# Kernel optimization log

Hardware: AMD Instinct MI355X
Metric: run time of the kernel (lower is better)

The kernel has to match this reference:

```python
import jax, jax.numpy as jnp
import numpy as np

BN_EPS = 1e-5
LEAKY_SLOPE = 0.1


def conv_bn_leaky(x, w, gamma, beta, mean, var, pad):
    # Conv2d(no bias) + BatchNorm2d(inference) + LeakyReLU(0.1), NCHW/OIHW
    y = jax.lax.conv_general_dilated(
        x, w, window_strides=(1, 1), padding=[(pad, pad), (pad, pad)],
        dimension_numbers=("NCHW", "OIHW", "NCHW"))
    scale = gamma / jnp.sqrt(var + BN_EPS)
    shift = beta - mean * scale
    y = y * scale[None, :, None, None] + shift[None, :, None, None]
    return jnp.where(y > 0, y, LEAKY_SLOPE * y)


def reorg(x, s=2):
    # vedanet Reorg: out[b, (a*s+d)*C + c, i, j] = x[b, c, i*s+a, j*s+d]
    B, C, H, W = x.shape
    Ho, Wo = H // s, W // s
    return x.reshape(B, C, Ho, s, Wo, s).transpose(0, 3, 5, 1, 2, 4).reshape(B, s * s * C, Ho, Wo)


def setup_inputs() -> dict:
    key = jax.random.key(0)
    ks = jax.random.split(key, 10)
    B, H, W = 32, 19, 19
    NC, NA = 20, 5
    return {
        "stage6": jax.random.normal(ks[0], (B, 1024, H, W), jnp.float32),
        "stage5": jax.random.normal(ks[1], (B, 512, 2 * H, 2 * W), jnp.float32),
        "w1": jax.random.normal(ks[2], (64, 512, 1, 1), jnp.float32) * 0.05,
        "g1": jnp.ones((64,), jnp.float32),
        "b1": jnp.zeros((64,), jnp.float32),
        "m1": jax.random.normal(ks[3], (64,), jnp.float32) * 0.1,
        "v1": jax.random.uniform(ks[4], (64,), jnp.float32, 0.5, 1.5),
        "w2": jax.random.normal(ks[5], (1024, 1280, 3, 3), jnp.float32) * 0.02,
        "g2": jnp.ones((1024,), jnp.float32),
        "b2": jnp.zeros((1024,), jnp.float32),
        "m2": jax.random.normal(ks[6], (1024,), jnp.float32) * 0.1,
        "v2": jax.random.uniform(ks[7], (1024,), jnp.float32, 0.5, 1.5),
        "meta_state": jax.random.normal(ks[8], (NC, NA * 6, 1025), jnp.float32) * 0.05,
    }


def reference(stage6, stage5, w1, g1, b1, m1, v1, w2, g2, b2, m2, v2, meta_state):
    # layers[0]: 1x1 conv-bn-leaky on stage5, then Reorg(2) -> (B, 256, H, W)
    x = conv_bn_leaky(stage5, w1, g1, b1, m1, v1, pad=0)
    x = reorg(x, 2)
    # layers[1]: 3x3 conv-bn-leaky on concat -> (B, 1024, H, W)
    pre = conv_bn_leaky(jnp.concatenate([x, stage6], axis=1), w2, g2, b2, m2, v2, pad=1)
    # meta_predict: per-class 1x1 conv, batched as one einsum
    cls_w = meta_state[:, :, :-1]   # (NC, NA*6, 1024)
    cls_b = meta_state[:, :, -1]    # (NC, NA*6)
    out = jnp.einsum("bkij,cmk->bcmij", pre, cls_w) + cls_b[None, :, :, None, None]
    B, NC, M = pre.shape[0], meta_state.shape[0], meta_state.shape[1]
    return out.reshape(B * NC, M, pre.shape[2], pre.shape[3])
```

## Files before the change

### kernel.cpp

```cpp
#include <hip/hip_runtime.h>

typedef unsigned short u16;
typedef unsigned int   u32;

typedef __attribute__((ext_vector_type(8))) short bf16x8;
typedef __attribute__((ext_vector_type(4))) float f32x4;

__device__ __forceinline__ u16 f2bf(float f) {
  u32 u = __float_as_uint(f);
  u32 r = (u + 0x7fffu + ((u >> 16) & 1u)) >> 16;
  return (u16)r;
}

__device__ __forceinline__ void async16(const void* g, void* l) {
  __builtin_amdgcn_global_load_lds(
      (const __attribute__((address_space(1))) u32*)g,
      (__attribute__((address_space(3))) u32*)l, 16, 0, 0);
}

__global__ __launch_bounds__(256) void mega_prep_kern(
    const float* __restrict__ stage5, const float* __restrict__ s6,
    const float* __restrict__ w1,
    const float* __restrict__ g1, const float* __restrict__ b1,
    const float* __restrict__ m1, const float* __restrict__ v1,
    const float* __restrict__ w2, const float* __restrict__ g2,
    const float* __restrict__ b2, const float* __restrict__ m2,
    const float* __restrict__ v2, const float* __restrict__ meta,
    u16* __restrict__ in_bf, u16* __restrict__ w2p,
    u16* __restrict__ clsp, float* __restrict__ clsb,
    float* __restrict__ shift2)
{
  __shared__ __align__(16) char smem[18816];
  const int bid = blockIdx.x;
  const int t = threadIdx.x;

  if (bid < 722) {
    float* sc_s = (float*)smem;
    float* sh_s = (float*)(smem + 256);
    char*  aT   = smem + 512;
    char*  bT   = smem + 4608;
    const int w = t >> 6, lane = t & 63;
    if (t < 64) {
      float s = g1[t] * rsqrtf(v1[t] + 1e-5f);
      sc_s[t] = s;
      sh_s[t] = b1[t] - m1[t] * s;
    }
    const int m0 = bid * 64;
    const int pS = t & 63, gS = t >> 6;
    const int mS = m0 + pS;
    const int bS = mS / 1444, hwS = mS - bS * 1444;
    const float* s5 = stage5 + (size_t)bS * (512 * 1444) + hwS;
    const int ocA = t >> 2, icqA = t & 3;
    const float* w1r = w1 + (size_t)ocA * 512 + icqA * 8;
    char* aW = aT + (ocA >> 4) * 1024 + (icqA * 16 + (ocA & 15)) * 16;
    char* bW = bT + pS * 64 + ((gS ^ ((pS >> 1) & 3))) * 16;
    const int bR = (w * 16 + (lane & 15)) * 64 +
                   (((lane >> 4) ^ (((lane & 15) >> 1) & 3))) * 16;
    f32x4 acc[4] = {};
    __syncthreads();
    const float sA = sc_s[ocA];
    for (int kc = 0; kc < 16; ++kc) {
      const int ic0 = kc * 32;
      float a8[8], b8[8];
#pragma unroll
      for (int e = 0; e < 8; ++e) a8[e] = w1r[ic0 + e];
#pragma unroll
      for (int e = 0; e < 8; ++e) b8[e] = s5[(size_t)(ic0 + gS * 8 + e) * 1444];
      __syncthreads();
      uint4 av, bv;
      av.x = (u32)f2bf(a8[0] * sA) | ((u32)f2bf(a8[1] * sA) << 16);
      av.y = (u32)f2bf(a8[2] * sA) | ((u32)f2bf(a8[3] * sA) << 16);
      av.z = (u32)f2bf(a8[4] * sA) | ((u32)f2bf(a8[5] * sA) << 16);
      av.w = (u32)f2bf(a8[6] * sA) | ((u32)f2bf(a8[7] * sA) << 16);
      bv.x = (u32)f2bf(b8[0]) | ((u32)f2bf(b8[1]) << 16);
      bv.y = (u32)f2bf(b8[2]) | ((u32)f2bf(b8[3]) << 16);
      bv.z = (u32)f2bf(b8[4]) | ((u32)f2bf(b8[5]) << 16);
      bv.w = (u32)f2bf(b8[6]) | ((u32)f2bf(b8[7]) << 16);
      *(uint4*)aW = av;
      *(uint4*)bW = bv;
      __syncthreads();
      bf16x8 bfv = *(const bf16x8*)(bT + bR);
#pragma unroll
      for (int i = 0; i < 4; ++i) {
        bf16x8 af = *(const bf16x8*)(aT + i * 1024 + lane * 16);
        acc[i] = __builtin_amdgcn_mfma_f32_16x16x32_bf16(af, bfv, acc[i], 0, 0, 0);
      }
    }
    const int mE = m0 + w * 16 + (lane & 15);
    const int bE = mE / 1444, hwE = mE - bE * 1444;
    const int h = hwE / 38, wq = hwE - h * 38;
    const int ho = h >> 1, wo = wq >> 1, q = ((h & 1) << 1) | (wq & 1);
    u16* dst = in_bf + (((size_t)bE * 21 + 1 + ho) * 21 + 1 + wo) * 1280 + q * 64;
    const int lq = lane >> 4;
#pragma unroll
    for (int i = 0; i < 4; ++i) {
      int oc = i * 16 + lq * 4;
      float v0 = acc[i][0] + sh_s[oc + 0]; v0 = v0 > 0.f ? v0 : 0.1f * v0;
      float v1_ = acc[i][1] + sh_s[oc + 1]; v1_ = v1_ > 0.f ? v1_ : 0.1f * v1_;
      float v2_ = acc[i][2] + sh_s[oc + 2]; v2_ = v2_ > 0.f ? v2_ : 0.1f * v2_;
      float v3 = acc[i][3] + sh_s[oc + 3]; v3 = v3 > 0.f ? v3 : 0.1f * v3;
      u32 lo = (u32)f2bf(v0) | ((u32)f2bf(v1_) << 16);
      u32 hi = (u32)f2bf(v2_) | ((u32)f2bf(v3) << 16);
      u32* dp = (u32*)(dst + oc);
      dp[0] = lo; dp[1] = hi;
    }
    return;
  }

  if (bid < 3794) {
    u16 (*tile)[66] = (u16(*)[66])smem;
    const int sub = bid - 722;
    const int jt = sub % 6, ct = (sub / 6) % 16, b = sub / 96;
    const int ij0 = jt * 64, c0 = ct * 64;
    const int col = t & 63, rr = t >> 6;
#pragma unroll
    for (int r = 0; r < 16; ++r) {
      int cl = r * 4 + rr;
      int ij = ij0 + col;
      float v = 0.f;
      if (ij < 361) v = s6[((size_t)b * 1024 + c0 + cl) * 361 + ij];
      tile[cl][col] = f2bf(v);
    }
    __syncthreads();
#pragma unroll
    for (int r = 0; r < 16; ++r) {
      int ijl = r * 4 + rr;
      int ij = ij0 + ijl;
      if (ij < 361) {
        int i = ij / 19, j = ij - i * 19;
        in_bf[(((size_t)b * 21 + 1 + i) * 21 + 1 + j) * 1280 + 256 + c0 + col] =
            tile[col][ijl];
      }
    }
    return;
  }

  if (bid < 5394) {
    int gi = (bid - 3794) * 256 + t;
    int b = gi / 12800;
    int rem = gi - b * 12800;
    int p = rem / 160, qq = rem - p * 160;
    int row, col;
    if (p < 21)      { row = 0;      col = p; }
    else if (p < 42) { row = 20;     col = p - 21; }
    else if (p < 61) { row = p - 41; col = 0; }
    else             { row = p - 60; col = 20; }
    uint4 z = {0u, 0u, 0u, 0u};
    *(uint4*)(in_bf + (((size_t)b * 21 + row) * 21 + col) * 1280 + qq * 8) = z;
    return;
  }

  if (bid < 5694) {
    int idx = (bid - 5394) * 256 + t;
    int cm = idx >> 7, a = idx & 127;
    int kc = a >> 2, ksub = a & 3;
    int tile_ = cm >> 7, g = (cm >> 4) & 7, mm = cm & 15;
    const float* srcp = meta + (size_t)cm * 1025 + a * 8;
    uint4 v;
    v.x = (u32)f2bf(srcp[0]) | ((u32)f2bf(srcp[1]) << 16);
    v.y = (u32)f2bf(srcp[2]) | ((u32)f2bf(srcp[3]) << 16);
    v.z = (u32)f2bf(srcp[4]) | ((u32)f2bf(srcp[5]) << 16);
    v.w = (u32)f2bf(srcp[6]) | ((u32)f2bf(srcp[7]) << 16);
    size_t dst = (((size_t)tile_ * 32 + kc) * 8 + g) * 512
                 + (size_t)(ksub * 16 + mm) * 8;
    *(uint4*)(clsp + dst) = v;
    if (idx < 600) clsb[idx] = meta[(size_t)idx * 1025 + 1024];
    if (idx < 1024) {
      float sc = g2[idx] * rsqrtf(v2[idx] + 1e-5f);
      shift2[idx] = b2[idx] - m2[idx] * sc;
    }
    return;
  }

  {
    u16* tile = (u16*)smem;
    float* sc_s = (float*)(smem + 18720);
    const int sub = bid - 5694;
    const int icb = sub % 10;
    const int oc0 = (sub / 10) * 8;
    if (t < 8) sc_s[t] = g2[oc0 + t] * rsqrtf(v2[oc0 + t] + 1e-5f);
    __syncthreads();
    const float* src = w2 + (size_t)oc0 * 11520 + (size_t)icb * 128 * 9;
#pragma unroll
    for (int r = 0; r < 36; ++r) {
      int p = r * 256 + t;
      int oc_l = p / 1152, rem = p - oc_l * 1152;
      int ic_l = rem / 9, khw = rem - ic_l * 9;
      tile[oc_l * 1170 + khw * 130 + ic_l] =
          f2bf(src[(size_t)oc_l * 11520 + rem] * sc_s[oc_l]);
    }
    __syncthreads();
#pragma unroll
    for (int r = 0; r < 5; ++r) {
      int wi = r * 256 + t;
      if (wi < 1152) {
        int oc_l = wi / 144, q = wi - oc_l * 144;
        int khw = q >> 4, c = (q >> 2) & 3, ksub = q & 3;
        int oc = oc0 + oc_l;
        int kt = khw * 40 + icb * 4 + c;
        const u16* s = &tile[oc_l * 1170 + khw * 130 + c * 32 + ksub * 8];
        uint4 v;
        v.x = (u32)s[0] | ((u32)s[1] << 16);
        v.y = (u32)s[2] | ((u32)s[3] << 16);
        v.z = (u32)s[4] | ((u32)s[5] << 16);
        v.w = (u32)s[6] | ((u32)s[7] << 16);
        size_t dst = (((size_t)(oc >> 8) * 360 + kt) * 2 + ((oc & 255) >> 7)) * 4096
                     + (size_t)(((oc >> 4) & 7) * 64 + ksub * 16 + (oc & 15)) * 8;
        *(uint4*)(w2p + dst) = v;
      }
    }
  }
}

__global__ __launch_bounds__(512, 2) void conv2_gemm_kern(
    const u16* __restrict__ Wp, const u16* __restrict__ Ig,
    const float* __restrict__ shift2, u16* __restrict__ pre)
{
  __shared__ u16 As[2][16384];
  __shared__ u16 Bs[2][12288];
  __shared__ float shft[256];

  const int t = threadIdx.x;
  const int w = t >> 6, lane = t & 63;
  const int wm = w >> 2, wn = w & 3;

  const int xcd = blockIdx.x & 7, sub8 = blockIdx.x >> 3;
  const int s = (xcd < 4 ? xcd * 31 : 124 + (xcd - 4) * 30) + sub8;
  const int mTile = s >> 2, ocTile = s & 3;
  const int m0 = mTile * 192, oc0 = ocTile * 256;

  const int rw = t >> 2;
  const int rpart = ((t & 3) ^ ((t >> 3) & 3)) * 8;
  int mA = m0 + rw;        if (mA > 11551) mA = 11551;
  int mB = m0 + 128 + rw;  if (mB > 11551) mB = 11551;
  const int bA = mA / 361, ijA = mA - bA * 361;
  const int ohA = ijA / 19, owA = ijA - ohA * 19;
  const int bB = mB / 361, ijB = mB - bB * 361;
  const int ohB = ijB / 19, owB = ijB - ohB * 19;
  const u16* pI0 = Ig + (size_t)((bA * 21 + ohA) * 21 + owA) * 1280 + rpart;
  const u16* pI1 = Ig + (size_t)((bB * 21 + ohB) * 21 + owB) * 1280 + rpart;

  const u16* pW = Wp + (size_t)ocTile * 2949120 + (size_t)t * 8;

  const int aOff = wm * 4096 + lane * 8;
  const int bOff = (wn * 48 + (lane & 15)) * 32 +
                   (((lane >> 4) ^ ((lane >> 1) & 3)) * 8);

  async16(pW,                 &As[0][t * 8]);
  async16(pW + 4096,          &As[0][4096 + t * 8]);
  async16(pW + 8192,          &As[0][8192 + t * 8]);
  async16(pW + 12288,         &As[0][12288 + t * 8]);
  async16(pI0,                &Bs[0][t * 8]);
  if (w < 4) async16(pI1,     &Bs[0][4096 + t * 8]);
  async16(pI0 + 32,           &Bs[0][6144 + t * 8]);
  if (w < 4) async16(pI1 + 32,&Bs[0][10240 + t * 8]);
  asm volatile("s_waitcnt vmcnt(0)" ::: "memory");
  __builtin_amdgcn_s_barrier();

  int skh = 0, skw = 0, sp = 1, sIo = 64;

  f32x4 acc[8][3] = {};

  for (int kq = 0; kq < 90; ++kq) {
#pragma unroll
    for (int r = 0; r < 2; ++r) {
      const int kt = kq * 2 + r;
      const int cur = r, nxt = r ^ 1;
      const int st = (kt < 179) ? kt + 1 : 179;
      const size_t aSrc = (size_t)st * 16384;

      bf16x8 a0[4], a1[4], bf[3];

#pragma unroll
      for (int i = 0; i < 4; ++i)
        a0[i] = *(const bf16x8*)&As[cur][aOff + i * 512];
#pragma unroll
      for (int j = 0; j < 3; ++j)
        bf[j] = *(const bf16x8*)&Bs[cur][bOff + j * 512];
      async16(pW + aSrc,        &As[nxt][t * 8]);
      async16(pW + aSrc + 4096, &As[nxt][4096 + t * 8]);
      async16(pI0 + sIo,        &Bs[nxt][t * 8]);
      if (w < 4) async16(pI1 + sIo, &Bs[nxt][4096 + t * 8]);
#pragma unroll
      for (int i = 0; i < 4; ++i)
        a1[i] = *(const bf16x8*)&As[cur][aOff + 2048 + i * 512];

      asm volatile("s_waitcnt lgkmcnt(4)" ::: "memory");
      __builtin_amdgcn_sched_barrier(0);
      __builtin_amdgcn_s_setprio(1);
#pragma unroll
      for (int i = 0; i < 4; ++i)
#pragma unroll
        for (int j = 0; j < 3; ++j)
          acc[i][j] = __builtin_amdgcn_mfma_f32_16x16x32_bf16(
              a0[i], bf[j], acc[i][j], 0, 0, 0);
      __builtin_amdgcn_s_setprio(0);

      asm volatile("s_waitcnt lgkmcnt(0)" ::: "memory");
      __builtin_amdgcn_sched_barrier(0);
      __builtin_amdgcn_s_setprio(1);
#pragma unroll
      for (int i = 0; i < 4; ++i)
#pragma unroll
        for (int j = 0; j < 3; ++j)
          acc[4 + i][j] = __builtin_amdgcn_mfma_f32_16x16x32_bf16(
              a1[i], bf[j], acc[4 + i][j], 0, 0, 0);
      __builtin_amdgcn_s_setprio(0);

#pragma unroll
      for (int i = 0; i < 4; ++i)
        a0[i] = *(const bf16x8*)&As[cur][8192 + aOff + i * 512];
#pragma unroll
      for (int j = 0; j < 3; ++j)
        bf[j] = *(const bf16x8*)&Bs[cur][6144 + bOff + j * 512];
      async16(pW + aSrc + 8192,  &As[nxt][8192 + t * 8]);
      async16(pW + aSrc + 12288, &As[nxt][12288 + t * 8]);
      async16(pI0 + sIo + 32,    &Bs[nxt][6144 + t * 8]);
      if (w < 4) async16(pI1 + sIo + 32, &Bs[nxt][10240 + t * 8]);
#pragma unroll
      for (int i = 0; i < 4; ++i)
        a1[i] = *(const bf16x8*)&As[cur][8192 + 2048 + aOff + i * 512];

      asm volatile("s_waitcnt lgkmcnt(4)" ::: "memory");
      __builtin_amdgcn_sched_barrier(0);
      __builtin_amdgcn_s_setprio(1);
#pragma unroll
      for (int i = 0; i < 4; ++i)
#pragma unroll
        for (int j = 0; j < 3; ++j)
          acc[i][j] = __builtin_amdgcn_mfma_f32_16x16x32_bf16(
              a0[i], bf[j], acc[i][j], 0, 0, 0);
      __builtin_amdgcn_s_setprio(0);

      asm volatile("s_waitcnt lgkmcnt(0)" ::: "memory");
      __builtin_amdgcn_sched_barrier(0);
      __builtin_amdgcn_s_setprio(1);
#pragma unroll
      for (int i = 0; i < 4; ++i)
#pragma unroll
        for (int j = 0; j < 3; ++j)
          acc[4 + i][j] = __builtin_amdgcn_mfma_f32_16x16x32_bf16(
              a1[i], bf[j], acc[4 + i][j], 0, 0, 0);
      __builtin_amdgcn_s_setprio(0);

      asm volatile("s_waitcnt vmcnt(0)" ::: "memory");
      __builtin_amdgcn_s_barrier();

      ++sp; sIo += 64;
      if (sp == 20) { sp = 0; ++skw; if (skw == 3) { skw = 0; ++skh; }
                      sIo = (skh * 21 + skw) * 1280; }
    }
  }

  if (t < 256) shft[t] = shift2[oc0 + t];
  __syncthreads();

  const int lq = lane >> 4, lr = lane & 15;
#pragma unroll
  for (int j = 0; j < 3; ++j) {
    const int m = m0 + wn * 48 + j * 16 + lr;
    if (m >= 11552) continue;
    u16* prow = pre + (size_t)m * 1024 + oc0 + wm * 128;
#pragma unroll
    for (int i = 0; i < 8; ++i) {
      const int ocl = i * 16 + lq * 4;
      float v0 = acc[i][j][0] + shft[wm * 128 + ocl + 0]; v0 = v0 > 0.f ? v0 : 0.1f * v0;
      float v1 = acc[i][j][1] + shft[wm * 128 + ocl + 1]; v1 = v1 > 0.f ? v1 : 0.1f * v1;
      float v2 = acc[i][j][2] + shft[wm * 128 + ocl + 2]; v2 = v2 > 0.f ? v2 : 0.1f * v2;
      float v3 = acc[i][j][3] + shft[wm * 128 + ocl + 3]; v3 = v3 > 0.f ? v3 : 0.1f * v3;
      u32 lo = (u32)f2bf(v0) | ((u32)f2bf(v1) << 16);
      u32 hi = (u32)f2bf(v2) | ((u32)f2bf(v3) << 16);
      u32* dp = (u32*)(prow + ocl);
      dp[0] = lo; dp[1] = hi;
    }
  }
}

__global__ __launch_bounds__(512) void einsum_gemm_kern(
    const u16* __restrict__ Ap, const u16* __restrict__ Bg,
    const float* __restrict__ biasg, float* __restrict__ out)
{
  __shared__ u16 Wa[3][4096];
  __shared__ u16 Ib[3][8192];
  __shared__ float sbias[128];
  const int t = threadIdx.x;
  const int w = t >> 6, lane = t & 63;
  const int q = w >> 1, ch = w & 1;
  const int m0 = blockIdx.x * 256;
  const int cm0 = blockIdx.y * 128;
  if (t < 128) { int c = cm0 + t; sbias[t] = (c < 600) ? biasg[c] : 0.f; }

  const u16* pA = Ap + (size_t)(cm0 >> 7) * (32 * 4096) + (size_t)t * 8;

  const int rw = t >> 2;
  const int rpart = ((t & 3) ^ ((t >> 3) & 3)) * 8;
  int rB0 = m0 + rw;        if (rB0 > 11551) rB0 = 11551;
  int rB1 = m0 + 128 + rw;  if (rB1 > 11551) rB1 = 11551;
  const u16* pB0 = Bg + (size_t)rB0 * 1024 + rpart;
  const u16* pB1 = Bg + (size_t)rB1 * 1024 + rpart;

  const int aBase = ch * 2048 + lane * 8;
  const int bBase = (q * 64 + (lane & 15)) * 32 +
                    (((lane >> 4) ^ ((lane >> 1) & 3))) * 8;

#pragma unroll
  for (int st = 0; st < 2; ++st) {
    const size_t off = (size_t)st * 32;
    async16(pA + (size_t)st * 4096, &Wa[st][t * 8]);
    async16(pB0 + off, &Ib[st][t * 8]);
    async16(pB1 + off, &Ib[st][4096 + t * 8]);
  }
  asm volatile("s_waitcnt vmcnt(3)" ::: "memory");
  __builtin_amdgcn_s_barrier();

  f32x4 acc[4][4] = {};

  for (int kt = 0; kt < 32; ++kt) {
    const int cb = kt % 3;
    const int stb = (kt + 2) % 3;
    const int st = (kt < 30) ? kt + 2 : 31;
    const size_t off = (size_t)st * 32;
    async16(pA + (size_t)st * 4096, &Wa[stb][t * 8]);
    async16(pB0 + off, &Ib[stb][t * 8]);
    async16(pB1 + off, &Ib[stb][4096 + t * 8]);

    bf16x8 af[4], bfv[4];
#pragma unroll
    for (int i = 0; i < 4; ++i)
      af[i] = *(const bf16x8*)&Wa[cb][aBase + i * 512];
#pragma unroll
    for (int j = 0; j < 4; ++j)
      bfv[j] = *(const bf16x8*)&Ib[cb][bBase + j * 512];
    asm volatile("s_waitcnt lgkmcnt(0)" ::: "memory");
    __builtin_amdgcn_sched_barrier(0);
    __builtin_amdgcn_s_setprio(1);
#pragma unroll
    for (int i = 0; i < 4; ++i)
#pragma unroll
      for (int j = 0; j < 4; ++j)
        acc[i][j] = __builtin_amdgcn_mfma_f32_16x16x32_bf16(
            af[i], bfv[j], acc[i][j], 0, 0, 0);
    __builtin_amdgcn_s_setprio(0);
    asm volatile("s_waitcnt vmcnt(3)" ::: "memory");
    __builtin_amdgcn_s_barrier();
  }

  const int lq = lane >> 4, lr = lane & 15;
#pragma unroll
  for (int j = 0; j < 4; ++j) {
    int m = m0 + q * 64 + j * 16 + lr;
    if (m >= 11552) continue;
    int b = m / 361, ij = m - b * 361;
    float* obase = out + (size_t)b * 216600 + ij;
#pragma unroll
    for (int i = 0; i < 4; ++i) {
      int cml = ch * 64 + i * 16 + lq * 4;
#pragma unroll
      for (int r = 0; r < 4; ++r) {
        int cm = cm0 + cml + r;
        if (cm < 600) obase[(size_t)cm * 361] = acc[i][j][r] + sbias[cml + r];
      }
    }
  }
}

extern "C" void kernel_launch(void* const* d_in, const int* in_sizes, int n_in,
                              void* d_out, int out_size, void* d_ws, size_t ws_size,
                              hipStream_t stream)
{
  const float* stage6 = (const float*)d_in[0];
  const float* stage5 = (const float*)d_in[1];
  const float* w1 = (const float*)d_in[2];
  const float* g1 = (const float*)d_in[3];
  const float* b1 = (const float*)d_in[4];
  const float* m1 = (const float*)d_in[5];
  const float* v1 = (const float*)d_in[6];
  const float* w2 = (const float*)d_in[7];
  const float* g2 = (const float*)d_in[8];
  const float* b2 = (const float*)d_in[9];
  const float* m2 = (const float*)d_in[10];
  const float* v2 = (const float*)d_in[11];
  const float* meta = (const float*)d_in[12];
  float* out = (float*)d_out;

  char* ws = (char*)d_ws;
  u16*   in_bf  = (u16*)(ws);
  u16*   w2p    = (u16*)(ws + 36126720);
  u16*   prebf  = (u16*)(ws + 59719680);
  u16*   clsp   = (u16*)(ws + 83378176);
  float* clsb   = (float*)(ws + 84688896);
  float* shift2 = (float*)(ws + 84691456);

  mega_prep_kern<<<6974, 256, 0, stream>>>(
      stage5, stage6, w1, g1, b1, m1, v1, w2, g2, b2, m2, v2, meta,
      in_bf, w2p, clsp, clsb, shift2);
  conv2_gemm_kern<<<244, 512, 0, stream>>>(w2p, in_bf, shift2, prebf);
  einsum_gemm_kern<<<dim3(46, 5), 512, 0, stream>>>(clsp, prebf, clsb, out);
}
```

Before: 520.5 us.

## Halve conv2 GEMM block to 256 threads with larger per-wave 128x96 tiles

The conv2 implicit-GEMM kernel now runs with 4 waves per block instead of 8, and each wave computes a 128x96 output sub-tile (8x6 MFMA accumulators) instead of 128x48. The loads that fill LDS are rearranged so 256 threads cover the same 256x192 block tile, with three B-row pointers per thread. The goal is more MFMA work per LDS fragment read and less wave-level overhead. The cost is a much larger accumulator register footprint, only one block per CU, and fewer waves available to hide latency.

```diff
diff --git a/kernel.cpp b/kernel.cpp
--- a/kernel.cpp
+++ b/kernel.cpp
@@ -212,7 +212,7 @@
   }
 }
 
-__global__ __launch_bounds__(512, 2) void conv2_gemm_kern(
+__global__ __launch_bounds__(256, 1) void conv2_gemm_kern(
     const u16* __restrict__ Wp, const u16* __restrict__ Ig,
     const float* __restrict__ shift2, u16* __restrict__ pre)
 {
@@ -222,7 +222,7 @@
 
   const int t = threadIdx.x;
   const int w = t >> 6, lane = t & 63;
-  const int wm = w >> 2, wn = w & 3;
+  const int wm = w >> 1, wn = w & 1;
 
   const int xcd = blockIdx.x & 7, sub8 = blockIdx.x >> 3;
   const int s = (xcd < 4 ? xcd * 31 : 124 + (xcd - 4) * 30) + sub8;
@@ -232,34 +232,39 @@
   const int rw = t >> 2;
   const int rpart = ((t & 3) ^ ((t >> 3) & 3)) * 8;
   int mA = m0 + rw;        if (mA > 11551) mA = 11551;
-  int mB = m0 + 128 + rw;  if (mB > 11551) mB = 11551;
+  int mB = m0 + 64 + rw;   if (mB > 11551) mB = 11551;
+  int mC = m0 + 128 + rw;  if (mC > 11551) mC = 11551;
   const int bA = mA / 361, ijA = mA - bA * 361;
   const int ohA = ijA / 19, owA = ijA - ohA * 19;
   const int bB = mB / 361, ijB = mB - bB * 361;
   const int ohB = ijB / 19, owB = ijB - ohB * 19;
-  const u16* pI0 = Ig + (size_t)((bA * 21 + ohA) * 21 + owA) * 1280 + rpart;
-  const u16* pI1 = Ig + (size_t)((bB * 21 + ohB) * 21 + owB) * 1280 + rpart;
+  const int bC = mC / 361, ijC = mC - bC * 361;
+  const int ohC = ijC / 19, owC = ijC - ohC * 19;
+  const u16* pIa = Ig + (size_t)((bA * 21 + ohA) * 21 + owA) * 1280 + rpart;
+  const u16* pIb = Ig + (size_t)((bB * 21 + ohB) * 21 + owB) * 1280 + rpart;
+  const u16* pIc = Ig + (size_t)((bC * 21 + ohC) * 21 + owC) * 1280 + rpart;
 
   const u16* pW = Wp + (size_t)ocTile * 2949120 + (size_t)t * 8;
 
   const int aOff = wm * 4096 + lane * 8;
-  const int bOff = (wn * 48 + (lane & 15)) * 32 +
+  const int bOff = (wn * 96 + (lane & 15)) * 32 +
                    (((lane >> 4) ^ ((lane >> 1) & 3)) * 8);
 
-  async16(pW,                 &As[0][t * 8]);
-  async16(pW + 4096,          &As[0][4096 + t * 8]);
-  async16(pW + 8192,          &As[0][8192 + t * 8]);
-  async16(pW + 12288,         &As[0][12288 + t * 8]);
-  async16(pI0,                &Bs[0][t * 8]);
-  if (w < 4) async16(pI1,     &Bs[0][4096 + t * 8]);
-  async16(pI0 + 32,           &Bs[0][6144 + t * 8]);
-  if (w < 4) async16(pI1 + 32,&Bs[0][10240 + t * 8]);
+#pragma unroll
+  for (int c = 0; c < 8; ++c)
+    async16(pW + c * 2048, &As[0][c * 2048 + t * 8]);
+  async16(pIa,      &Bs[0][t * 8]);
+  async16(pIb,      &Bs[0][2048 + t * 8]);
+  async16(pIc,      &Bs[0][4096 + t * 8]);
+  async16(pIa + 32, &Bs[0][6144 + t * 8]);
+  async16(pIb + 32, &Bs[0][8192 + t * 8]);
+  async16(pIc + 32, &Bs[0][10240 + t * 8]);
   asm volatile("s_waitcnt vmcnt(0)" ::: "memory");
   __builtin_amdgcn_s_barrier();
 
   int skh = 0, skw = 0, sp = 1, sIo = 64;
 
-  f32x4 acc[8][3] = {};
+  f32x4 acc[8][6] = {};
 
   for (int kq = 0; kq < 90; ++kq) {
 #pragma unroll
@@ -269,18 +274,21 @@
       const int st = (kt < 179) ? kt + 1 : 179;
       const size_t aSrc = (size_t)st * 16384;
 
-      bf16x8 a0[4], a1[4], bf[3];
-
+      bf16x8 a0[4], a1[4], bf[6];
+
+#pragma unroll
+      for (int j = 0; j < 6; ++j)
+        bf[j] = *(const bf16x8*)&Bs[cur][bOff + j * 512];
 #pragma unroll
       for (int i = 0; i < 4; ++i)
         a0[i] = *(const bf16x8*)&As[cur][aOff + i * 512];
-#pragma unroll
-      for (int j = 0; j < 3; ++j)
-        bf[j] = *(const bf16x8*)&Bs[cur][bOff + j * 512];
       async16(pW + aSrc,        &As[nxt][t * 8]);
+      async16(pW + aSrc + 2048, &As[nxt][2048 + t * 8]);
       async16(pW + aSrc + 4096, &As[nxt][4096 + t * 8]);
-      async16(pI0 + sIo,        &Bs[nxt][t * 8]);
-      if (w < 4) async16(pI1 + sIo, &Bs[nxt][4096 + t * 8]);
+      async16(pW + aSrc + 6144, &As[nxt][6144 + t * 8]);
+      async16(pIa + sIo, &Bs[nxt][t * 8]);
+      async16(pIb + sIo, &Bs[nxt][2048 + t * 8]);
+      async16(pIc + sIo, &Bs[nxt][4096 + t * 8]);
 #pragma unroll
       for (int i = 0; i < 4; ++i)
         a1[i] = *(const bf16x8*)&As[cur][aOff + 2048 + i * 512];
@@ -291,7 +299,7 @@
 #pragma unroll
       for (int i = 0; i < 4; ++i)
 #pragma unroll
-        for (int j = 0; j < 3; ++j)
+        for (int j = 0; j < 6; ++j)
           acc[i][j] = __builtin_amdgcn_mfma_f32_16x16x32_bf16(
               a0[i], bf[j], acc[i][j], 0, 0, 0);
       __builtin_amdgcn_s_setprio(0);
@@ -302,21 +310,24 @@
 #pragma unroll
       for (int i = 0; i < 4; ++i)
 #pragma unroll
-        for (int j = 0; j < 3; ++j)
+        for (int j = 0; j < 6; ++j)
           acc[4 + i][j] = __builtin_amdgcn_mfma_f32_16x16x32_bf16(
               a1[i], bf[j], acc[4 + i][j], 0, 0, 0);
       __builtin_amdgcn_s_setprio(0);
 
 #pragma unroll
+      for (int j = 0; j < 6; ++j)
+        bf[j] = *(const bf16x8*)&Bs[cur][6144 + bOff + j * 512];
+#pragma unroll
       for (int i = 0; i < 4; ++i)
         a0[i] = *(const bf16x8*)&As[cur][8192 + aOff + i * 512];
-#pragma unroll
-      for (int j = 0; j < 3; ++j)
-        bf[j] = *(const bf16x8*)&Bs[cur][6144 + bOff + j * 512];
       async16(pW + aSrc + 8192,  &As[nxt][8192 + t * 8]);
+      async16(pW + aSrc + 10240, &As[nxt][10240 + t * 8]);
       async16(pW + aSrc + 12288, &As[nxt][12288 + t * 8]);
-      async16(pI0 + sIo + 32,    &Bs[nxt][6144 + t * 8]);
-      if (w < 4) async16(pI1 + sIo + 32, &Bs[nxt][10240 + t * 8]);
+      async16(pW + aSrc + 14336, &As[nxt][14336 + t * 8]);
+      async16(pIa + sIo + 32, &Bs[nxt][6144 + t * 8]);
+      async16(pIb + sIo + 32, &Bs[nxt][8192 + t * 8]);
+      async16(pIc + sIo + 32, &Bs[nxt][10240 + t * 8]);
 #pragma unroll
       for (int i = 0; i < 4; ++i)
         a1[i] = *(const bf16x8*)&As[cur][8192 + 2048 + aOff + i * 512];
@@ -327,7 +338,7 @@
 #pragma unroll
       for (int i = 0; i < 4; ++i)
 #pragma unroll
-        for (int j = 0; j < 3; ++j)
+        for (int j = 0; j < 6; ++j)
           acc[i][j] = __builtin_amdgcn_mfma_f32_16x16x32_bf16(
               a0[i], bf[j], acc[i][j], 0, 0, 0);
       __builtin_amdgcn_s_setprio(0);
@@ -338,7 +349,7 @@
 #pragma unroll
       for (int i = 0; i < 4; ++i)
 #pragma unroll
-        for (int j = 0; j < 3; ++j)
+        for (int j = 0; j < 6; ++j)
           acc[4 + i][j] = __builtin_amdgcn_mfma_f32_16x16x32_bf16(
               a1[i], bf[j], acc[4 + i][j], 0, 0, 0);
       __builtin_amdgcn_s_setprio(0);
@@ -352,13 +363,13 @@
     }
   }
 
-  if (t < 256) shft[t] = shift2[oc0 + t];
+  shft[t] = shift2[oc0 + t];
   __syncthreads();
 
   const int lq = lane >> 4, lr = lane & 15;
 #pragma unroll
-  for (int j = 0; j < 3; ++j) {
-    const int m = m0 + wn * 48 + j * 16 + lr;
+  for (int j = 0; j < 6; ++j) {
+    const int m = m0 + wn * 96 + j * 16 + lr;
     if (m >= 11552) continue;
     u16* prow = pre + (size_t)m * 1024 + oc0 + wm * 128;
 #pragma unroll
@@ -494,6 +505,6 @@
   mega_prep_kern<<<6974, 256, 0, stream>>>(
       stage5, stage6, w1, g1, b1, m1, v1, w2, g2, b2, m2, v2, meta,
       in_bf, w2p, clsp, clsb, shift2);
-  conv2_gemm_kern<<<244, 512, 0, stream>>>(w2p, in_bf, shift2, prebf);
+  conv2_gemm_kern<<<244, 256, 0, stream>>>(w2p, in_bf, shift2, prebf);
   einsum_gemm_kern<<<dim3(46, 5), 512, 0, stream>>>(clsp, prebf, clsb, out);
 }
```

After: 611.0 us. +17.4%, slower.
